# Kernel tuning notes

Measured on AMD Instinct MI355X. Metric: run time of the kernel, lower is better.

The kernel has to match this reference:

```python
import jax, jax.numpy as jnp
import numpy as np

CLIP_LEN = 8      # == num_frame
NUM_NODES = 7     # == group_size
NUM_BASIC = 1024
NUM_MIXED = 8192
T = 2 * CLIP_LEN - 1          # 15 temporal offsets
N = 1 + NUM_NODES * CLIP_LEN  # 57 graph size


def setup_inputs() -> dict:
    key = jax.random.key(0)
    k1, k2, k3, k4 = jax.random.split(key, 4)
    mat = jax.random.normal(k1, (NUM_BASIC, NUM_NODES, NUM_NODES), dtype=jnp.float32)
    temp_extent = jax.random.normal(k2, (NUM_BASIC, T), dtype=jnp.float32)
    # nn.Linear(num_basic, num_mixed): weight [out,in], bias [out]
    W = jax.random.normal(k3, (NUM_MIXED, NUM_BASIC), dtype=jnp.float32) * (1.0 / np.sqrt(NUM_BASIC))
    b = jax.random.normal(k4, (NUM_MIXED,), dtype=jnp.float32) * 0.01
    return {"mat": mat, "temp_extent": temp_extent, "W": W, "b": b}


def reference(mat, temp_extent, W, b):
    n, cl = NUM_NODES, CLIP_LEN
    Hb = mat.shape[0]
    te = jax.nn.sigmoid(temp_extent) + 1.0                      # [Hb, T]
    x = jnp.einsum('ht,hnm->htmn', te, mat)                     # [Hb, T, n, n]
    x = jax.nn.relu(x)
    x = jnp.transpose(x, (1, 2, 3, 0)).reshape(T * n, n, Hb)    # (t m) n h
    y = x @ W.T + b                                             # [(t m), n, Hm]
    y = jax.nn.relu(jnp.transpose(y, (2, 1, 0)))                # [Hm, n, T*n]
    Hm = y.shape[0]
    # vectorized version of the per-frame slice-write loop:
    # frame i reads cols n*(cl-1-i) : n*(2*cl-1-i) of y
    starts = n * (cl - 1 - jnp.arange(cl))                      # [cl]
    idx = starts[:, None] + jnp.arange(n * cl)[None, :]         # [cl, n*cl]
    blocks = y[:, :, idx]                                       # [Hm, n, cl, n*cl]
    blocks = jnp.transpose(blocks, (0, 2, 1, 3)).reshape(Hm, n * cl, n * cl)
    base = jnp.zeros((Hm, N, N), dtype=y.dtype)
    base = base.at[:, 0::7, 0::7].set(1.0)                      # person-node anchors
    mixed = base.at[:, 1:, 1:].set(blocks)                      # [Hm, N, N]
    # degree normalization D^{-1/2} A D^{-1/2} (row sums, clamped at 1)
    d = jnp.clip(mixed.sum(axis=2), 1.0, None) ** -0.5          # [Hm, N]
    ret = d[:, :, None] * mixed * d[:, None, :]
    return ret
```

## Files before the change

### kernel.cpp

```cpp
#include <hip/hip_runtime.h>

#define HB 1024
#define HM 8192
#define NR 735
#define NPAD 768
#define NOUT 57

#define BM 64
#define BN 128
#define BK 32

typedef __attribute__((ext_vector_type(8))) _Float16 half8;
typedef __attribute__((ext_vector_type(4))) _Float16 half4v;
typedef __attribute__((ext_vector_type(4))) float floatx4;

__global__ __launch_bounds__(256) void prep_kernel(
    const float* __restrict__ mat, const float* __restrict__ tex,
    const float4* __restrict__ W,
    _Float16* __restrict__ Xh, half4v* __restrict__ Wh) {
  const int blk = blockIdx.x;
  if (blk < NPAD) {
    const int r = blk;
    const int n = r % 7;
    const int tm = r / 7;
    const int m = tm % 7;
    const int t = tm / 7;
#pragma unroll
    for (int i = 0; i < 4; ++i) {
      const int h = i * 256 + threadIdx.x;
      float v = 0.f;
      if (r < NR) {
        const float mv = mat[h * 49 + n * 7 + m];
        const float te = 1.f / (1.f + expf(-tex[h * 15 + t])) + 1.f;
        v = te * mv;
        v = v > 0.f ? v : 0.f;
      }
      Xh[r * HB + h] = (_Float16)v;
    }
  } else {
    const int idx = (blk - NPAD) * 256 + threadIdx.x;
    const float4 v = W[idx];
    half4v h;
    h.x = (_Float16)v.x;
    h.y = (_Float16)v.y;
    h.z = (_Float16)v.z;
    h.w = (_Float16)v.w;
    Wh[idx] = h;
  }
}

#define STAGE(p, k0)                                                           \
  do {                                                                         \
    const int arow_ = wave * 16 + srow;                                        \
    __builtin_amdgcn_global_load_lds(                                          \
        (const __attribute__((address_space(1))) void*)(                       \
            A + abase + (size_t)arow_ * HB + (k0) + skh),                      \
        (__attribute__((address_space(3))) void*)(&As[p][wave * 512]),         \
        16, 0, 0);                                                             \
    _Pragma("unroll")                                                          \
    for (int it_ = 0; it_ < 2; ++it_) {                                        \
      const int chunk_ = wave * 2 + it_;                                       \
      const int brow_ = chunk_ * 16 + srow;                                    \
      __builtin_amdgcn_global_load_lds(                                        \
          (const __attribute__((address_space(1))) void*)(                     \
              B + bbase + (size_t)brow_ * HB + (k0) + skh),                    \
          (__attribute__((address_space(3))) void*)(&Bs[p][chunk_ * 512]),     \
          16, 0, 0);                                                           \
    }                                                                          \
  } while (0)

__global__ __launch_bounds__(256) void gemm_kernel(
    const _Float16* __restrict__ A,
    const _Float16* __restrict__ B,
    const float* __restrict__ bias,
    float* __restrict__ Y) {
  __shared__ __align__(16) _Float16 As[2][BM * BK];
  __shared__ __align__(16) _Float16 Bs[2][BN * BK];

  const int tid = threadIdx.x;
  const int lane = tid & 63;
  const int wave = tid >> 6;

  const int bid = blockIdx.x;
  const int wg = (bid & 7) * 96 + (bid >> 3);
  const int bn = wg % 6;
  const int bm = wg / 6;

  const int wm = (wave >> 1) * 32;
  const int wn = (wave & 1) * 64;

  floatx4 acc[2][4] = {};

  const int srow = lane >> 2;
  const int skh = (lane & 3) * 8;
  const size_t abase = (size_t)(bm * BM) * HB;
  const size_t bbase = (size_t)(bn * BN) * HB;

  const int mrow = lane & 15;
  const int quad = lane >> 4;

  STAGE(0, 0);
  __syncthreads();

  int p = 0;
  for (int k0 = 0; k0 < HB; k0 += BK) {
    if (k0 + BK < HB) STAGE(p ^ 1, k0 + BK);

    half8 af[2], bf[4];
#pragma unroll
    for (int i = 0; i < 2; ++i)
      af[i] = *(const half8*)(&As[p][(wm + i * 16 + mrow) * BK + quad * 8]);
#pragma unroll
    for (int j = 0; j < 4; ++j)
      bf[j] = *(const half8*)(&Bs[p][(wn + j * 16 + mrow) * BK + quad * 8]);
#pragma unroll
    for (int i = 0; i < 2; ++i)
#pragma unroll
      for (int j = 0; j < 4; ++j)
        acc[i][j] =
            __builtin_amdgcn_mfma_f32_16x16x32_f16(af[i], bf[j], acc[i][j], 0, 0, 0);

    __syncthreads();
    p ^= 1;
  }

#pragma unroll
  for (int i = 0; i < 2; ++i) {
#pragma unroll
    for (int j = 0; j < 4; ++j) {
#pragma unroll
      for (int reg = 0; reg < 4; ++reg) {
        const int grow = bm * BM + wm + i * 16 + quad * 4 + reg;
        const int gcol = bn * BN + wn + j * 16 + mrow;
        float v = acc[i][j][reg] + bias[grow];
        v = v > 0.f ? v : 0.f;
        Y[(size_t)grow * NPAD + gcol] = v;
      }
    }
  }
}

__global__ __launch_bounds__(256) void epilogue_kernel(
    const float* __restrict__ Y, float* __restrict__ out) {
  const int j = blockIdx.x;
  __shared__ float ly[NR];
  __shared__ float dd[NOUT];

  const float* yj = Y + (size_t)j * NPAD;
  for (int i = threadIdx.x; i < NR; i += 256) ly[i] = yj[i];
  __syncthreads();

  if (threadIdx.x < 4 * NOUT) {
    const int r = threadIdx.x >> 2;
    const int sub = threadIdx.x & 3;
    float s = 0.f;
    if (r == 0) {
      s = (sub == 0) ? 9.f : 0.f;
    } else {
      const int c = (r - 1) / 7;
      const int n = (r - 1) % 7;
      const int base = 7 * (7 - c);
      if (sub == 0) s = (n == 6) ? 1.f : 0.f;
#pragma unroll
      for (int p = sub; p < 56; p += 4) s += ly[(base + p) * 7 + n];
    }
    s += __shfl_xor(s, 1);
    s += __shfl_xor(s, 2);
    if (sub == 0) {
      s = s < 1.f ? 1.f : s;
      dd[r] = rsqrtf(s);
    }
  }
  __syncthreads();

  float* oj = out + (size_t)j * (NOUT * NOUT);
  for (int i = threadIdx.x; i < NOUT * NOUT; i += 256) {
    const int r = i / NOUT;
    const int q = i % NOUT;
    float v;
    if (r == 0) {
      v = (q % 7 == 0) ? dd[0] * dd[q] : 0.f;
    } else {
      const int c = (r - 1) / 7;
      const int n = (r - 1) % 7;
      if (q == 0)
        v = (n == 6) ? dd[r] * dd[0] : 0.f;
      else
        v = dd[r] * ly[(7 * (7 - c) + q - 1) * 7 + n] * dd[q];
    }
    oj[i] = v;
  }
}

extern "C" void kernel_launch(void* const* d_in, const int* in_sizes, int n_in,
                              void* d_out, int out_size, void* d_ws, size_t ws_size,
                              hipStream_t stream) {
  const float* mat = (const float*)d_in[0];
  const float* tex = (const float*)d_in[1];
  const float* W = (const float*)d_in[2];
  const float* b = (const float*)d_in[3];
  float* out = (float*)d_out;

  char* ws = (char*)d_ws;
  _Float16* Xh = (_Float16*)(ws);
  _Float16* Wh = (_Float16*)(ws + (size_t)NPAD * HB * 2);
  float* Y = (float*)(ws + (size_t)NPAD * HB * 2 + (size_t)HM * HB * 2);

  prep_kernel<<<NPAD + HM * HB / 4 / 256, 256, 0, stream>>>(
      mat, tex, (const float4*)W, Xh, (half4v*)Wh);
  gemm_kernel<<<HM / BM * (NPAD / BN), 256, 0, stream>>>(Wh, Xh, b, Y);
  epilogue_kernel<<<HM, 256, 0, stream>>>(Y, out);
}
```

Before: 185.1 us.

## Fuse GEMM with degree-normalization epilogue using full-width N tiles in LDS

Result: slower. 214.2 us (+15.8%).

```diff
diff --git a/kernel.cpp b/kernel.cpp
--- a/kernel.cpp
+++ b/kernel.cpp
@@ -6,9 +6,12 @@
 #define NPAD 768
 #define NOUT 57
 
-#define BM 64
-#define BN 128
-#define BK 32
+#define FBM 32
+#define FBK 32
+#define NCHUNK 50
+#define YLSTRIDE 772
+
+#define SMEM_BYTES 106112
 
 typedef __attribute__((ext_vector_type(8))) _Float16 half8;
 typedef __attribute__((ext_vector_type(4))) _Float16 half4v;
@@ -49,74 +52,67 @@
   }
 }
 
-#define STAGE(p, k0)                                                           \
+#define STAGE(pp, k0)                                                          \
   do {                                                                         \
-    const int arow_ = wave * 16 + srow;                                        \
-    __builtin_amdgcn_global_load_lds(                                          \
-        (const __attribute__((address_space(1))) void*)(                       \
-            A + abase + (size_t)arow_ * HB + (k0) + skh),                      \
-        (__attribute__((address_space(3))) void*)(&As[p][wave * 512]),         \
-        16, 0, 0);                                                             \
     _Pragma("unroll")                                                          \
-    for (int it_ = 0; it_ < 2; ++it_) {                                        \
-      const int chunk_ = wave * 2 + it_;                                       \
-      const int brow_ = chunk_ * 16 + srow;                                    \
-      __builtin_amdgcn_global_load_lds(                                        \
-          (const __attribute__((address_space(1))) void*)(                     \
-              B + bbase + (size_t)brow_ * HB + (k0) + skh),                    \
-          (__attribute__((address_space(3))) void*)(&Bs[p][chunk_ * 512]),     \
-          16, 0, 0);                                                           \
+    for (int t_ = 0; t_ < 7; ++t_) {                                           \
+      const int c_ = wave + t_ * 8;                                            \
+      if (c_ < NCHUNK) {                                                       \
+        const bool isA_ = (c_ < 2);                                            \
+        const int row_ = (isA_ ? c_ : (c_ - 2)) * 16 + srow;                   \
+        const _Float16* gsrc_ =                                                \
+            isA_ ? (A + abase + (size_t)row_ * HB + (k0) + skh)                \
+                 : (B + (size_t)row_ * HB + (k0) + skh);                       \
+        char* ldst_ = isA_ ? (smem + (pp)*2048 + c_ * 1024)                    \
+                           : (smem + 4096 + (pp)*49152 + (c_ - 2) * 1024);     \
+        __builtin_amdgcn_global_load_lds(                                      \
+            (const __attribute__((address_space(1))) void*)gsrc_,              \
+            (__attribute__((address_space(3))) void*)ldst_, 16, 0, 0);         \
+      }                                                                        \
     }                                                                          \
   } while (0)
 
-__global__ __launch_bounds__(256) void gemm_kernel(
+__global__ __launch_bounds__(512) void fused_kernel(
     const _Float16* __restrict__ A,
     const _Float16* __restrict__ B,
     const float* __restrict__ bias,
-    float* __restrict__ Y) {
-  __shared__ __align__(16) _Float16 As[2][BM * BK];
-  __shared__ __align__(16) _Float16 Bs[2][BN * BK];
+    float* __restrict__ out) {
+  __shared__ __align__(16) char smem[SMEM_BYTES];
 
   const int tid = threadIdx.x;
   const int lane = tid & 63;
   const int wave = tid >> 6;
-
-  const int bid = blockIdx.x;
-  const int wg = (bid & 7) * 96 + (bid >> 3);
-  const int bn = wg % 6;
-  const int bm = wg / 6;
-
-  const int wm = (wave >> 1) * 32;
-  const int wn = (wave & 1) * 64;
-
-  floatx4 acc[2][4] = {};
+  const int blk = blockIdx.x;
 
   const int srow = lane >> 2;
   const int skh = (lane & 3) * 8;
-  const size_t abase = (size_t)(bm * BM) * HB;
-  const size_t bbase = (size_t)(bn * BN) * HB;
+  const size_t abase = (size_t)(blk * FBM) * HB;
 
   const int mrow = lane & 15;
   const int quad = lane >> 4;
 
+  floatx4 acc[2][6] = {};
+
   STAGE(0, 0);
   __syncthreads();
 
   int p = 0;
-  for (int k0 = 0; k0 < HB; k0 += BK) {
-    if (k0 + BK < HB) STAGE(p ^ 1, k0 + BK);
-
-    half8 af[2], bf[4];
+  for (int k0 = 0; k0 < HB; k0 += FBK) {
+    if (k0 + FBK < HB) STAGE(p ^ 1, k0 + FBK);
+
+    const _Float16* Asp = (const _Float16*)(smem + p * 2048);
+    const _Float16* Bsp = (const _Float16*)(smem + 4096 + p * 49152);
+    half8 af[2], bf[6];
 #pragma unroll
     for (int i = 0; i < 2; ++i)
-      af[i] = *(const half8*)(&As[p][(wm + i * 16 + mrow) * BK + quad * 8]);
-#pragma unroll
-    for (int j = 0; j < 4; ++j)
-      bf[j] = *(const half8*)(&Bs[p][(wn + j * 16 + mrow) * BK + quad * 8]);
+      af[i] = *(const half8*)(Asp + (i * 16 + mrow) * FBK + quad * 8);
+#pragma unroll
+    for (int j = 0; j < 6; ++j)
+      bf[j] = *(const half8*)(Bsp + (wave * 96 + j * 16 + mrow) * FBK + quad * 8);
 #pragma unroll
     for (int i = 0; i < 2; ++i)
 #pragma unroll
-      for (int j = 0; j < 4; ++j)
+      for (int j = 0; j < 6; ++j)
         acc[i][j] =
             __builtin_amdgcn_mfma_f32_16x16x32_f16(af[i], bf[j], acc[i][j], 0, 0, 0);
 
@@ -124,71 +120,69 @@
     p ^= 1;
   }
 
+  float* Yl = (float*)smem;
+  float* ddl = (float*)(smem + 98816);
 #pragma unroll
   for (int i = 0; i < 2; ++i) {
 #pragma unroll
-    for (int j = 0; j < 4; ++j) {
+    for (int jf = 0; jf < 6; ++jf) {
 #pragma unroll
       for (int reg = 0; reg < 4; ++reg) {
-        const int grow = bm * BM + wm + i * 16 + quad * 4 + reg;
-        const int gcol = bn * BN + wn + j * 16 + mrow;
-        float v = acc[i][j][reg] + bias[grow];
-        v = v > 0.f ? v : 0.f;
-        Y[(size_t)grow * NPAD + gcol] = v;
+        const int jrow = i * 16 + quad * 4 + reg;
+        const int col = wave * 96 + jf * 16 + mrow;
+        float v = acc[i][jf][reg] + bias[blk * FBM + jrow];
+        Yl[jrow * YLSTRIDE + col] = v > 0.f ? v : 0.f;
       }
     }
   }
-}
-
-__global__ __launch_bounds__(256) void epilogue_kernel(
-    const float* __restrict__ Y, float* __restrict__ out) {
-  const int j = blockIdx.x;
-  __shared__ float ly[NR];
-  __shared__ float dd[NOUT];
-
-  const float* yj = Y + (size_t)j * NPAD;
-  for (int i = threadIdx.x; i < NR; i += 256) ly[i] = yj[i];
   __syncthreads();
 
-  if (threadIdx.x < 4 * NOUT) {
-    const int r = threadIdx.x >> 2;
-    const int sub = threadIdx.x & 3;
-    float s = 0.f;
+  for (int pr = tid; pr < FBM * NOUT; pr += 512) {
+    const int jj = pr / NOUT;
+    const int r = pr % NOUT;
+    float s;
     if (r == 0) {
-      s = (sub == 0) ? 9.f : 0.f;
+      s = 9.f;
     } else {
       const int c = (r - 1) / 7;
       const int n = (r - 1) % 7;
       const int base = 7 * (7 - c);
-      if (sub == 0) s = (n == 6) ? 1.f : 0.f;
-#pragma unroll
-      for (int p = sub; p < 56; p += 4) s += ly[(base + p) * 7 + n];
-    }
-    s += __shfl_xor(s, 1);
-    s += __shfl_xor(s, 2);
-    if (sub == 0) {
-      s = s < 1.f ? 1.f : s;
-      dd[r] = rsqrtf(s);
-    }
+      s = (n == 6) ? 1.f : 0.f;
+      const float* lyj = Yl + jj * YLSTRIDE;
+#pragma unroll
+      for (int q = 0; q < 56; ++q) s += lyj[(base + q) * 7 + n];
+    }
+    s = s < 1.f ? 1.f : s;
+    ddl[jj * NOUT + r] = rsqrtf(s);
   }
   __syncthreads();
 
-  float* oj = out + (size_t)j * (NOUT * NOUT);
-  for (int i = threadIdx.x; i < NOUT * NOUT; i += 256) {
-    const int r = i / NOUT;
-    const int q = i % NOUT;
-    float v;
-    if (r == 0) {
-      v = (q % 7 == 0) ? dd[0] * dd[q] : 0.f;
-    } else {
-      const int c = (r - 1) / 7;
-      const int n = (r - 1) % 7;
-      if (q == 0)
-        v = (n == 6) ? dd[r] * dd[0] : 0.f;
-      else
-        v = dd[r] * ly[(7 * (7 - c) + q - 1) * 7 + n] * dd[q];
-    }
-    oj[i] = v;
+  float* ob = out + (size_t)blk * FBM * (NOUT * NOUT);
+  for (int v4 = tid; v4 < FBM * NOUT * NOUT / 4; v4 += 512) {
+    float4 o;
+#pragma unroll
+    for (int e = 0; e < 4; ++e) {
+      const int f = v4 * 4 + e;
+      const int jj = f / (NOUT * NOUT);
+      const int rem = f - jj * (NOUT * NOUT);
+      const int r = rem / NOUT;
+      const int q = rem - r * NOUT;
+      const float* lyj = Yl + jj * YLSTRIDE;
+      const float* dj = ddl + jj * NOUT;
+      float val;
+      if (r == 0) {
+        val = (q % 7 == 0) ? dj[0] * dj[q] : 0.f;
+      } else {
+        const int c = (r - 1) / 7;
+        const int n = (r - 1) % 7;
+        if (q == 0)
+          val = (n == 6) ? dj[r] * dj[0] : 0.f;
+        else
+          val = dj[r] * lyj[(7 * (7 - c) + q - 1) * 7 + n] * dj[q];
+      }
+      (&o.x)[e] = val;
+    }
+    ((float4*)ob)[v4] = o;
   }
 }
 
@@ -204,10 +198,8 @@
   char* ws = (char*)d_ws;
   _Float16* Xh = (_Float16*)(ws);
   _Float16* Wh = (_Float16*)(ws + (size_t)NPAD * HB * 2);
-  float* Y = (float*)(ws + (size_t)NPAD * HB * 2 + (size_t)HM * HB * 2);
 
   prep_kernel<<<NPAD + HM * HB / 4 / 256, 256, 0, stream>>>(
       mat, tex, (const float4*)W, Xh, (half4v*)Wh);
-  gemm_kernel<<<HM / BM * (NPAD / BN), 256, 0, stream>>>(Wh, Xh, b, Y);
-  epilogue_kernel<<<HM, 256, 0, stream>>>(Y, out);
+  fused_kernel<<<HM / FBM, 512, 0, stream>>>(Wh, Xh, b, out);
 }
```

## Double GEMM K-tile to 64 and batch four rows per epilogue block with float4 stores

Applied to the files above, without the earlier changes.

Result: no change. 187.1 us (+1.1%).

```diff
diff --git a/kernel.cpp b/kernel.cpp
--- a/kernel.cpp
+++ b/kernel.cpp
@@ -8,7 +8,7 @@
 
 #define BM 64
 #define BN 128
-#define BK 32
+#define BK 64
 
 typedef __attribute__((ext_vector_type(8))) _Float16 half8;
 typedef __attribute__((ext_vector_type(4))) _Float16 half4v;
@@ -49,22 +49,28 @@
   }
 }
 
-#define STAGE(p, k0)                                                           \
+#define STAGE(pp, k0)                                                          \
   do {                                                                         \
-    const int arow_ = wave * 16 + srow;                                        \
-    __builtin_amdgcn_global_load_lds(                                          \
-        (const __attribute__((address_space(1))) void*)(                       \
-            A + abase + (size_t)arow_ * HB + (k0) + skh),                      \
-        (__attribute__((address_space(3))) void*)(&As[p][wave * 512]),         \
-        16, 0, 0);                                                             \
     _Pragma("unroll")                                                          \
     for (int it_ = 0; it_ < 2; ++it_) {                                        \
-      const int chunk_ = wave * 2 + it_;                                       \
-      const int brow_ = chunk_ * 16 + srow;                                    \
+      const int c_ = wave * 2 + it_;                                           \
+      const int row_ = ((c_ & 3) * 16) + srow;                                 \
+      const int kof_ = ((c_ >> 2) * 32) + skh;                                 \
       __builtin_amdgcn_global_load_lds(                                        \
           (const __attribute__((address_space(1))) void*)(                     \
-              B + bbase + (size_t)brow_ * HB + (k0) + skh),                    \
-          (__attribute__((address_space(3))) void*)(&Bs[p][chunk_ * 512]),     \
+              A + abase + (size_t)row_ * HB + (k0) + kof_),                    \
+          (__attribute__((address_space(3))) void*)(&As[pp][c_ * 512 + lane * 8]), \
+          16, 0, 0);                                                           \
+    }                                                                          \
+    _Pragma("unroll")                                                          \
+    for (int it_ = 0; it_ < 4; ++it_) {                                        \
+      const int c_ = wave * 4 + it_;                                           \
+      const int row_ = ((c_ & 7) * 16) + srow;                                 \
+      const int kof_ = ((c_ >> 3) * 32) + skh;                                 \
+      __builtin_amdgcn_global_load_lds(                                        \
+          (const __attribute__((address_space(1))) void*)(                     \
+              B + bbase + (size_t)row_ * HB + (k0) + kof_),                    \
+          (__attribute__((address_space(3))) void*)(&Bs[pp][c_ * 512 + lane * 8]), \
           16, 0, 0);                                                           \
     }                                                                          \
   } while (0)
@@ -106,19 +112,26 @@
   for (int k0 = 0; k0 < HB; k0 += BK) {
     if (k0 + BK < HB) STAGE(p ^ 1, k0 + BK);
 
-    half8 af[2], bf[4];
-#pragma unroll
-    for (int i = 0; i < 2; ++i)
-      af[i] = *(const half8*)(&As[p][(wm + i * 16 + mrow) * BK + quad * 8]);
-#pragma unroll
-    for (int j = 0; j < 4; ++j)
-      bf[j] = *(const half8*)(&Bs[p][(wn + j * 16 + mrow) * BK + quad * 8]);
-#pragma unroll
-    for (int i = 0; i < 2; ++i)
+    half8 af[2][2], bf[2][4];
+#pragma unroll
+    for (int s = 0; s < 2; ++s) {
+#pragma unroll
+      for (int i = 0; i < 2; ++i)
+        af[s][i] =
+            *(const half8*)(&As[p][s * 2048 + (wm + i * 16 + mrow) * 32 + quad * 8]);
 #pragma unroll
       for (int j = 0; j < 4; ++j)
-        acc[i][j] =
-            __builtin_amdgcn_mfma_f32_16x16x32_f16(af[i], bf[j], acc[i][j], 0, 0, 0);
+        bf[s][j] =
+            *(const half8*)(&Bs[p][s * 4096 + (wn + j * 16 + mrow) * 32 + quad * 8]);
+    }
+#pragma unroll
+    for (int s = 0; s < 2; ++s)
+#pragma unroll
+      for (int i = 0; i < 2; ++i)
+#pragma unroll
+        for (int j = 0; j < 4; ++j)
+          acc[i][j] = __builtin_amdgcn_mfma_f32_16x16x32_f16(af[s][i], bf[s][j],
+                                                             acc[i][j], 0, 0, 0);
 
     __syncthreads();
     p ^= 1;
@@ -142,53 +155,62 @@
 
 __global__ __launch_bounds__(256) void epilogue_kernel(
     const float* __restrict__ Y, float* __restrict__ out) {
-  const int j = blockIdx.x;
-  __shared__ float ly[NR];
-  __shared__ float dd[NOUT];
-
-  const float* yj = Y + (size_t)j * NPAD;
-  for (int i = threadIdx.x; i < NR; i += 256) ly[i] = yj[i];
+  const int j0 = blockIdx.x * 4;
+  __shared__ float ly[4][NR];
+  __shared__ float dd[4][NOUT];
+
+#pragma unroll
+  for (int jj = 0; jj < 4; ++jj)
+    for (int i = threadIdx.x; i < NR; i += 256)
+      ly[jj][i] = Y[(size_t)(j0 + jj) * NPAD + i];
   __syncthreads();
 
   if (threadIdx.x < 4 * NOUT) {
-    const int r = threadIdx.x >> 2;
-    const int sub = threadIdx.x & 3;
-    float s = 0.f;
+    const int jj = threadIdx.x / NOUT;
+    const int r = threadIdx.x % NOUT;
+    float s;
     if (r == 0) {
-      s = (sub == 0) ? 9.f : 0.f;
+      s = 9.f;
     } else {
       const int c = (r - 1) / 7;
       const int n = (r - 1) % 7;
       const int base = 7 * (7 - c);
-      if (sub == 0) s = (n == 6) ? 1.f : 0.f;
-#pragma unroll
-      for (int p = sub; p < 56; p += 4) s += ly[(base + p) * 7 + n];
-    }
-    s += __shfl_xor(s, 1);
-    s += __shfl_xor(s, 2);
-    if (sub == 0) {
-      s = s < 1.f ? 1.f : s;
-      dd[r] = rsqrtf(s);
-    }
+      s = (n == 6) ? 1.f : 0.f;
+      const float* lyj = ly[jj];
+#pragma unroll
+      for (int q = 0; q < 56; ++q) s += lyj[(base + q) * 7 + n];
+    }
+    s = s < 1.f ? 1.f : s;
+    dd[jj][r] = rsqrtf(s);
   }
   __syncthreads();
 
-  float* oj = out + (size_t)j * (NOUT * NOUT);
-  for (int i = threadIdx.x; i < NOUT * NOUT; i += 256) {
-    const int r = i / NOUT;
-    const int q = i % NOUT;
-    float v;
-    if (r == 0) {
-      v = (q % 7 == 0) ? dd[0] * dd[q] : 0.f;
-    } else {
-      const int c = (r - 1) / 7;
-      const int n = (r - 1) % 7;
-      if (q == 0)
-        v = (n == 6) ? dd[r] * dd[0] : 0.f;
-      else
-        v = dd[r] * ly[(7 * (7 - c) + q - 1) * 7 + n] * dd[q];
-    }
-    oj[i] = v;
+  float4* ob = (float4*)(out + (size_t)j0 * (NOUT * NOUT));
+  for (int v4 = threadIdx.x; v4 < NOUT * NOUT; v4 += 256) {
+    float4 o;
+#pragma unroll
+    for (int e = 0; e < 4; ++e) {
+      const int f = v4 * 4 + e;
+      const int jj = f / (NOUT * NOUT);
+      const int rem = f - jj * (NOUT * NOUT);
+      const int r = rem / NOUT;
+      const int q = rem - r * NOUT;
+      const float* lyj = ly[jj];
+      const float* dj = dd[jj];
+      float val;
+      if (r == 0) {
+        val = (q % 7 == 0) ? dj[0] * dj[q] : 0.f;
+      } else {
+        const int c = (r - 1) / 7;
+        const int n = (r - 1) % 7;
+        if (q == 0)
+          val = (n == 6) ? dj[r] * dj[0] : 0.f;
+        else
+          val = dj[r] * lyj[(7 * (7 - c) + q - 1) * 7 + n] * dj[q];
+      }
+      (&o.x)[e] = val;
+    }
+    ob[v4] = o;
   }
 }
 
@@ -209,5 +231,5 @@
   prep_kernel<<<NPAD + HM * HB / 4 / 256, 256, 0, stream>>>(
       mat, tex, (const float4*)W, Xh, (half4v*)Wh);
   gemm_kernel<<<HM / BM * (NPAD / BN), 256, 0, stream>>>(Wh, Xh, b, Y);
-  epilogue_kernel<<<HM, 256, 0, stream>>>(Y, out);
-}
+  epilogue_kernel<<<HM / 4, 256, 0, stream>>>(Y, out);
+}
```
